# Kernel tuning notes

Measured on AMD Instinct MI355X. Metric: run time of the kernel, lower is better.

Reference implementation:

```python
import jax, jax.numpy as jnp
import numpy as np

L, P = 16384, 512
DT_MIN, DT_MAX = 0.001, 0.1
THRESHOLD = 1.0  # spike threshold assumed for cartesian_spike


def setup_inputs() -> dict:
    key = jax.random.key(0)
    k1, k2, k3, k4, k5, k6 = jax.random.split(key, 6)
    u = jax.random.normal(k1, (L, P), dtype=jnp.float32)
    # Stored Lambda param: [..., 0] = log(-Re(Lambda)) with Re(Lambda) < 0, [..., 1] = Im(Lambda)
    lam_real_neg = jax.random.uniform(k2, (P,), minval=0.1, maxval=1.0)  # -Re(Lambda)
    lam_imag = jax.random.normal(k3, (P,)) * 3.0
    Lambda = jnp.stack([jnp.log(lam_real_neg), lam_imag], axis=-1).astype(jnp.float32)
    # init_log_steps: log(dt) uniform in [log(dt_min), log(dt_max)], shape (P, 1)
    log_step = (np.log(DT_MIN) + jax.random.uniform(k4, (P, 1)) * (np.log(DT_MAX) - np.log(DT_MIN))).astype(jnp.float32)
    V_re = jax.random.normal(k5, (P, P), dtype=jnp.float32) / np.sqrt(P)
    V_im = jax.random.normal(k6, (P, P), dtype=jnp.float32) / np.sqrt(P)
    return {"u": u, "Lambda": Lambda, "log_step": log_step, "V_re": V_re, "V_im": V_im}


def _binop(q_i, q_j):
    A_i, b_i = q_i
    A_j, b_j = q_j
    return (A_j * A_i, A_j * b_i + b_j)


def reference(u, Lambda, log_step, V_re, V_im):
    # keep_imag = False: u stays real. discretization = 'zoh', activation = 'cartesian_spike'.
    Lambda_tilde = -jnp.exp(Lambda[..., 0]) + 1j * Lambda[..., 1]            # (P,) complex
    step = jnp.exp(log_step[:, 0])                                            # (P,)
    Lambda_bar = jnp.exp(Lambda_tilde * step)                                 # (P,) |.|<1
    # B_tilde = I, so zoh gives B_bar = diag((Lambda_bar - 1)/Lambda); B_bar @ u_t = coef * u_t
    B_coef = (Lambda_bar - 1.0) / Lambda_tilde                                # (P,)
    Lambda_elements = jnp.broadcast_to(Lambda_bar, (u.shape[0], Lambda_bar.shape[0]))
    Bu_elements = B_coef[None, :] * u.astype(Lambda_bar.dtype)                # (L, P) complex
    _, xs = jax.lax.associative_scan(_binop, (Lambda_elements, Bu_elements))  # (L, P)
    V = V_re + 1j * V_im
    xs = xs @ V.T                                                             # vmap(V @ x) over L
    spikes = (xs.real > THRESHOLD).astype(jnp.float32)                        # cartesian_spike
    return spikes
```

## Files before the change

### kernel.cpp

```cpp
#include <hip/hip_runtime.h>

#define L_LEN   16384
#define P_DIM   512
#define CHUNK   32
#define NCHUNK  512

#define KDIM    1024
#define NDIM    512
#define BM      64
#define NBLK    (L_LEN / BM)

typedef __bf16 bf16_t;
typedef __bf16 bf16x8 __attribute__((ext_vector_type(8)));
typedef float  floatx4 __attribute__((ext_vector_type(4)));

__device__ __forceinline__ uint32_t pack_bf16(float a, float b) {
    bf16_t ha = (bf16_t)a, hb = (bf16_t)b;
    return (uint32_t)__builtin_bit_cast(unsigned short, ha)
         | ((uint32_t)__builtin_bit_cast(unsigned short, hb) << 16);
}

__device__ __forceinline__ void ch_consts(float lam0, float lam1, float ls,
                                          float& ar, float& ai,
                                          float& br, float& bi) {
    float lr = -expf(lam0);
    float li = lam1;
    float s  = expf(ls);
    float er = expf(lr * s);
    ar = er * cosf(li * s);
    ai = er * sinf(li * s);
    float dr = ar - 1.0f, di = ai;
    float inv = 1.0f / (lr * lr + li * li);
    br = (dr * lr + di * li) * inv;
    bi = (di * lr - dr * li) * inv;
}

__global__ void __launch_bounds__(256) k_scan_ends(const float* __restrict__ u,
        const float* __restrict__ Lam, const float* __restrict__ lstep,
        const float* __restrict__ Vre, const float* __restrict__ Vim,
        float2* __restrict__ endv, bf16_t* __restrict__ Bt) {
    const int t = threadIdx.x;
    const int c = blockIdx.x;

    {
        int idx = c * 256 + t;
        float2 vr = ((const float2*)Vre)[idx];
        float2 vi = ((const float2*)Vim)[idx];
        ((uint2*)Bt)[idx] = make_uint2(pack_bf16(vr.x, -vi.x),
                                       pack_bf16(vr.y, -vi.y));
    }

    float4 lam4 = ((const float4*)Lam)[t];
    float2 ls2  = ((const float2*)lstep)[t];
    float ar0, ai0, br0, bi0, ar1, ai1, br1, bi1;
    ch_consts(lam4.x, lam4.y, ls2.x, ar0, ai0, br0, bi0);
    ch_consts(lam4.z, lam4.w, ls2.y, ar1, ai1, br1, bi1);

    float xr0 = 0.f, xi0 = 0.f, xr1 = 0.f, xi1 = 0.f;
    const float2* up = (const float2*)(u + (size_t)c * CHUNK * P_DIM) + t;
    #pragma unroll 8
    for (int k = 0; k < CHUNK; ++k) {
        float2 uv = up[(size_t)k * (P_DIM / 2)];
        float nr0 = ar0 * xr0 - ai0 * xi0 + br0 * uv.x;
        float ni0 = ar0 * xi0 + ai0 * xr0 + bi0 * uv.x;
        float nr1 = ar1 * xr1 - ai1 * xi1 + br1 * uv.y;
        float ni1 = ar1 * xi1 + ai1 * xr1 + bi1 * uv.y;
        xr0 = nr0; xi0 = ni0; xr1 = nr1; xi1 = ni1;
    }
    ((float4*)endv)[c * 256 + t] = make_float4(xr0, xi0, xr1, xi1);
}

__global__ void __launch_bounds__(1024) k_carry(const float* __restrict__ Lam,
        const float* __restrict__ lstep, const float2* __restrict__ endv,
        float2* __restrict__ carry) {
    __shared__ float2 zl[NCHUNK * 2];
    const int tid = threadIdx.x;
    const int g = tid & 1;
    const int c = tid >> 1;
    const int p = blockIdx.x * 2 + g;

    float lr = -expf(Lam[2 * p + 0]);
    float li = Lam[2 * p + 1];
    float s  = expf(lstep[p]);
    float tt = s * (float)CHUNK;
    float er = expf(lr * tt);
    float Ar = er * cosf(li * tt);
    float Ai = er * sinf(li * tt);

    float2 e = endv[(size_t)c * P_DIM + p];
    float zr = e.x, zi = e.y;
    zl[c * 2 + g] = make_float2(zr, zi);
    __syncthreads();
    for (int st = 1; st < NCHUNK; st <<= 1) {
        float tr = 0.f, ti = 0.f;
        if (c >= st) { float2 v = zl[(c - st) * 2 + g]; tr = v.x; ti = v.y; }
        __syncthreads();
        zr += Ar * tr - Ai * ti;
        zi += Ar * ti + Ai * tr;
        zl[c * 2 + g] = make_float2(zr, zi);
        float nAr = Ar * Ar - Ai * Ai;
        float nAi = 2.f * Ar * Ai;
        Ar = nAr; Ai = nAi;
        __syncthreads();
    }
    float2 cv = make_float2(0.f, 0.f);
    if (c > 0) cv = zl[(c - 1) * 2 + g];
    carry[(size_t)c * P_DIM + p] = cv;
}

__global__ void __launch_bounds__(512, 2) k_scan_gemm(const float* __restrict__ u,
        const float* __restrict__ Lam, const float* __restrict__ lstep,
        const float2* __restrict__ carry, const bf16_t* __restrict__ Bt,
        float* __restrict__ out) {
    __shared__ bf16_t As[BM * KDIM];

    const int tid = threadIdx.x;
    const int c   = blockIdx.x;

    {
        const int p = tid;
        float ar, ai, br, bi;
        ch_consts(Lam[2 * p + 0], Lam[2 * p + 1], lstep[p], ar, ai, br, bi);
        float2 cv = carry[(size_t)(2 * c) * P_DIM + p];
        float xr = cv.x, xi = cv.y;
        const float* up = u + (size_t)c * BM * P_DIM + p;
        const int ct  = p >> 2;
        const int sub = (p & 3) * 4;
        #pragma unroll 4
        for (int k = 0; k < BM; ++k) {
            float uv = up[(size_t)k * P_DIM];
            float nr = ar * xr - ai * xi + br * uv;
            float ni = ar * xi + ai * xr + bi * uv;
            xr = nr; xi = ni;
            int st = ct ^ (k & 7);
            *(uint32_t*)((char*)As + (size_t)k * 2048 + st * 16 + sub)
                = pack_bf16(xr, xi);
        }
    }
    __syncthreads();

    const int lane = tid & 63;
    const int w    = tid >> 6;
    const int wn   = w * 64;
    const int fr_m = lane & 15;
    const int fr_g = lane >> 4;

    floatx4 acc[4][4];
    #pragma unroll
    for (int i = 0; i < 4; ++i)
        #pragma unroll
        for (int j = 0; j < 4; ++j) {
            floatx4 z = {0.f, 0.f, 0.f, 0.f};
            acc[i][j] = z;
        }

    const bf16_t* Bw = Bt + (size_t)(wn + fr_m) * KDIM + fr_g * 8;

    #pragma unroll 2
    for (int kt = 0; kt < KDIM; kt += 32) {
        bf16x8 af[4], bf[4];
        #pragma unroll
        for (int j = 0; j < 4; ++j)
            bf[j] = *(const bf16x8*)(Bw + (size_t)j * 16 * KDIM + kt);
        #pragma unroll
        for (int i = 0; i < 4; ++i) {
            int m  = i * 16 + fr_m;
            int cc = (kt >> 3) + fr_g;
            int sc = cc ^ (m & 7);
            af[i] = *(const bf16x8*)((const char*)As + (size_t)m * 2048 + sc * 16);
        }
        #pragma unroll
        for (int i = 0; i < 4; ++i)
            #pragma unroll
            for (int j = 0; j < 4; ++j)
                acc[i][j] = __builtin_amdgcn_mfma_f32_16x16x32_bf16(
                    af[i], bf[j], acc[i][j], 0, 0, 0);
    }

    float* outb = out + (size_t)c * BM * NDIM;
    #pragma unroll
    for (int i = 0; i < 4; ++i)
        #pragma unroll
        for (int j = 0; j < 4; ++j)
            #pragma unroll
            for (int r = 0; r < 4; ++r) {
                int rr = i * 16 + fr_g * 4 + r;
                int cl = wn + j * 16 + fr_m;
                float v = acc[i][j][r];
                outb[(size_t)rr * NDIM + cl] = (v > 1.0f) ? 1.0f : 0.0f;
            }
}

extern "C" void kernel_launch(void* const* d_in, const int* in_sizes, int n_in,
                              void* d_out, int out_size, void* d_ws, size_t ws_size,
                              hipStream_t stream) {
    (void)in_sizes; (void)n_in; (void)out_size; (void)ws_size;
    const float* u     = (const float*)d_in[0];
    const float* Lam   = (const float*)d_in[1];
    const float* lstep = (const float*)d_in[2];
    const float* Vre   = (const float*)d_in[3];
    const float* Vim   = (const float*)d_in[4];
    float* out = (float*)d_out;

    char* ws = (char*)d_ws;
    const size_t endv_bytes  = (size_t)NCHUNK * P_DIM * sizeof(float2);
    const size_t carry_bytes = endv_bytes;
    float2* endv  = (float2*)(ws);
    float2* carry = (float2*)(ws + endv_bytes);
    bf16_t* Bt    = (bf16_t*)(ws + endv_bytes + carry_bytes);

    hipLaunchKernelGGL(k_scan_ends, dim3(NCHUNK), dim3(256), 0, stream,
                       u, Lam, lstep, Vre, Vim, endv, Bt);
    hipLaunchKernelGGL(k_carry, dim3(P_DIM / 2), dim3(1024), 0, stream,
                       Lam, lstep, endv, carry);
    hipLaunchKernelGGL(k_scan_gemm, dim3(NBLK), dim3(512), 0, stream,
                       u, Lam, lstep, carry, Bt, out);
}
```

Before: 135.8 us.

## Split scan-GEMM blocks into 32-row tiles with N halves for more parallelism

Shrinks the fused scan+GEMM row tile from 64 to 32 (matching the 32-step carry chunk) and splits the 512 output columns across two blocks, quadrupling the grid to 1024 blocks. Each warp now computes a 32x32 output tile instead of 64x64. The u loads are preloaded into registers ahead of the recurrence, and the LDS swizzle widens to 16. Both N-halves redundantly recompute the same sequential scan and re-read u. Lower per-warp MFMA reuse means more B-matrix traffic per output. Smaller shared memory and a launch bound of 4 aim for higher occupancy and latency hiding.

```diff
diff --git a/kernel.cpp b/kernel.cpp
--- a/kernel.cpp
+++ b/kernel.cpp
@@ -7,8 +7,9 @@
 
 #define KDIM    1024
 #define NDIM    512
-#define BM      64
-#define NBLK    (L_LEN / BM)
+#define BM      32
+#define NSPLIT  2
+#define NBLK    (L_LEN / BM * NSPLIT)
 
 typedef __bf16 bf16_t;
 typedef __bf16 bf16x8 __attribute__((ext_vector_type(8)));
@@ -108,84 +109,88 @@
     carry[(size_t)c * P_DIM + p] = cv;
 }
 
-__global__ void __launch_bounds__(512, 2) k_scan_gemm(const float* __restrict__ u,
+__global__ void __launch_bounds__(512, 4) k_scan_gemm(const float* __restrict__ u,
         const float* __restrict__ Lam, const float* __restrict__ lstep,
         const float2* __restrict__ carry, const bf16_t* __restrict__ Bt,
         float* __restrict__ out) {
     __shared__ bf16_t As[BM * KDIM];
 
     const int tid = threadIdx.x;
-    const int c   = blockIdx.x;
+    const int bx  = blockIdx.x;
+    const int c   = bx >> 1;
+    const int nh  = bx & 1;
 
     {
         const int p = tid;
         float ar, ai, br, bi;
         ch_consts(Lam[2 * p + 0], Lam[2 * p + 1], lstep[p], ar, ai, br, bi);
-        float2 cv = carry[(size_t)(2 * c) * P_DIM + p];
+        float2 cv = carry[(size_t)c * P_DIM + p];
         float xr = cv.x, xi = cv.y;
         const float* up = u + (size_t)c * BM * P_DIM + p;
+        float ur[BM];
+        #pragma unroll
+        for (int k = 0; k < BM; ++k) ur[k] = up[(size_t)k * P_DIM];
         const int ct  = p >> 2;
         const int sub = (p & 3) * 4;
-        #pragma unroll 4
+        #pragma unroll
         for (int k = 0; k < BM; ++k) {
-            float uv = up[(size_t)k * P_DIM];
-            float nr = ar * xr - ai * xi + br * uv;
-            float ni = ar * xi + ai * xr + bi * uv;
+            float nr = ar * xr - ai * xi + br * ur[k];
+            float ni = ar * xi + ai * xr + bi * ur[k];
             xr = nr; xi = ni;
-            int st = ct ^ (k & 7);
+            int st = ct ^ (k & 15);
             *(uint32_t*)((char*)As + (size_t)k * 2048 + st * 16 + sub)
                 = pack_bf16(xr, xi);
         }
     }
     __syncthreads();
 
-    const int lane = tid & 63;
-    const int w    = tid >> 6;
-    const int wn   = w * 64;
-    const int fr_m = lane & 15;
-    const int fr_g = lane >> 4;
-
-    floatx4 acc[4][4];
+    const int lane  = tid & 63;
+    const int w     = tid >> 6;
+    const int nbase = nh * 256 + w * 32;
+    const int fr_m  = lane & 15;
+    const int fr_g  = lane >> 4;
+
+    floatx4 acc[2][2];
     #pragma unroll
-    for (int i = 0; i < 4; ++i)
-        #pragma unroll
-        for (int j = 0; j < 4; ++j) {
+    for (int i = 0; i < 2; ++i)
+        #pragma unroll
+        for (int j = 0; j < 2; ++j) {
             floatx4 z = {0.f, 0.f, 0.f, 0.f};
             acc[i][j] = z;
         }
 
-    const bf16_t* Bw = Bt + (size_t)(wn + fr_m) * KDIM + fr_g * 8;
-
-    #pragma unroll 2
+    const bf16_t* Bw = Bt + (size_t)(nbase + fr_m) * KDIM + fr_g * 8;
+
+    #pragma unroll
     for (int kt = 0; kt < KDIM; kt += 32) {
-        bf16x8 af[4], bf[4];
-        #pragma unroll
-        for (int j = 0; j < 4; ++j)
-            bf[j] = *(const bf16x8*)(Bw + (size_t)j * 16 * KDIM + kt);
-        #pragma unroll
-        for (int i = 0; i < 4; ++i) {
+        bf16x8 af[2], bfv[2];
+        #pragma unroll
+        for (int j = 0; j < 2; ++j)
+            bfv[j] = *(const bf16x8*)(Bw + (size_t)j * 16 * KDIM + kt);
+        #pragma unroll
+        for (int i = 0; i < 2; ++i) {
             int m  = i * 16 + fr_m;
             int cc = (kt >> 3) + fr_g;
-            int sc = cc ^ (m & 7);
+            int sc = cc ^ (m & 15);
             af[i] = *(const bf16x8*)((const char*)As + (size_t)m * 2048 + sc * 16);
         }
         #pragma unroll
-        for (int i = 0; i < 4; ++i)
+        for (int i = 0; i < 2; ++i)
             #pragma unroll
-            for (int j = 0; j < 4; ++j)
+            for (int j = 0; j < 2; ++j)
                 acc[i][j] = __builtin_amdgcn_mfma_f32_16x16x32_bf16(
-                    af[i], bf[j], acc[i][j], 0, 0, 0);
+                    af[i], bfv[j], acc[i][j], 0, 0, 0);
     }
 
     float* outb = out + (size_t)c * BM * NDIM;
     #pragma unroll
-    for (int i = 0; i < 4; ++i)
-        #pragma unroll
-        for (int j = 0; j < 4; ++j)
+    for (int i = 0; i < 2; ++i)
+        #pragma unroll
+        for (int j = 0; j < 2; ++j)
             #pragma unroll
             for (int r = 0; r < 4; ++r) {
                 int rr = i * 16 + fr_g * 4 + r;
-                int cl = wn + j * 16 + fr_m;
+                int cl = nbase + j * 16 + fr_m;
                 float v = acc[i][j][r];
                 outb[(size_t)rr * NDIM + cl] = (v > 1.0f) ? 1.0f : 0.0f;
             }
```

New measurement: 161.3 us. 18.8% more time.
